# Optimization experiments

Hardware: AMD Instinct MI355X
Metric: run time of the kernel (lower is better)

Reference implementation:

```python
import jax, jax.numpy as jnp
import numpy as np

K, P, Q, D = 16, 1024, 1024, 64  # heads, value-in dim, out dim, head dim; P'=P, Q'=Q, D'=D
B, N = 2, 2048                   # batch, seq (self-attention: M=N)
TEMPERATURE = jnp.sqrt(jnp.float32(D))

def _xavier(key, shape):
    fan_in, fan_out = shape[-2], shape[-1]
    lim = jnp.sqrt(6.0 / (fan_in + fan_out))
    return jax.random.uniform(key, shape, jnp.float32, -lim, lim)

def setup_inputs() -> dict:
    key = jax.random.key(0)
    k0, k1, k2, k3, k4 = jax.random.split(key, 5)
    return {
        'y_prime': jax.random.normal(k0, (B, N, Q), jnp.float32),
        'mask': jnp.zeros((N, N), jnp.float32),  # log-domain additive mask [M,N]
        'Lam_x': _xavier(k1, (K, P, D)),  # Lambda^(x): [K,P',D']
        'Lam_y': _xavier(k2, (K, Q, D)),  # Lambda^(y): [K,Q',D']
        'Th_x': _xavier(k3, (K, P, D)),   # Theta^(x):  [K,P,D]
        'Th_y': _xavier(k4, (K, Q, D)),   # Theta^(y):  [K,Q,D]
    }

def reference(y_prime, mask, Lam_x, Lam_y, Th_x, Th_y):
    # self-attention: x' = x = y'
    x_p = y_prime
    x = x_p
    # key projection: [B,M,K,D']
    r = jnp.einsum('bmp,kpd->bmkd', x_p, Lam_x)
    # bilinear scores: [K,B,M,N]
    r = jnp.einsum('bmkd,kqd,bnq->kbmn', r, Lam_y, y_prime)
    r = r + mask[None, None, :, :]
    # softmax over M (axis=-2), scaled by sqrt(D')
    A = jax.nn.softmax(r / TEMPERATURE, axis=-2)
    # value aggregation: [B,N,K,D]
    r = jnp.einsum('kbmn,bmp,kpd->bnkd', A, x, Th_x)
    # output projection: [B,N,Q]
    return jnp.einsum('bnkd,kqd->bnq', r, Th_y)
```

## Files before the change

### kernel.cpp

```cpp
#include <hip/hip_runtime.h>
#include <hip/hip_bf16.h>

#define KH 16
#define PD 1024
#define QD 1024
#define DD 64
#define BB 2
#define NN 2048
#define BN 4096
#define ST 72
#define SOFT_C 12.0f

typedef unsigned short u16;
typedef __attribute__((ext_vector_type(8))) short bf16x8;
typedef __attribute__((ext_vector_type(4))) short bf16x4;
typedef __attribute__((ext_vector_type(4))) float f32x4;

__device__ __forceinline__ float bf2f(u16 u) {
    return __uint_as_float(((unsigned)u) << 16);
}
__device__ __forceinline__ u16 f2bf(float f) {
    unsigned x = __float_as_uint(f);
    x += 0x7FFFu + ((x >> 16) & 1u);
    return (u16)(x >> 16);
}
__device__ __forceinline__ f32x4 mfma_k32(bf16x8 a, bf16x8 b, f32x4 c) {
    return __builtin_amdgcn_mfma_f32_16x16x32_bf16(a, b, c, 0, 0, 0);
}
__device__ __forceinline__ f32x4 mfma_k16(bf16x4 a, bf16x4 b, f32x4 c) {
#if __has_builtin(__builtin_amdgcn_mfma_f32_16x16x16bf16_1k)
    return __builtin_amdgcn_mfma_f32_16x16x16bf16_1k(a, b, c, 0, 0, 0);
#else
    asm("v_mfma_f32_16x16x16_bf16 %0, %1, %2, %0" : "+v"(c) : "v"(a), "v"(b));
    return c;
#endif
}
__device__ __forceinline__ bf16x8 ldfrag(const u16* base, int r0, int kc, int lane) {
    return *reinterpret_cast<const bf16x8*>(base + (r0 + (lane & 15)) * ST + kc +
                                            ((lane >> 4) << 3));
}
__device__ __forceinline__ bf16x4 ldfrag4(const u16* base, int r0, int kc, int lane) {
    return *reinterpret_cast<const bf16x4*>(base + (r0 + (lane & 15)) * ST + kc +
                                            ((lane >> 4) << 2));
}
__device__ __forceinline__ bf16x8 ldfragL(const u16* base, int r0, int kc, int lane) {
    return *reinterpret_cast<const bf16x8*>(base + ((r0 + (lane & 15)) << 6) + kc +
                                            ((lane >> 4) << 3));
}
__device__ __forceinline__ bf16x4 pack4(float a, float b, float c, float d) {
    union { bf16x4 v; __hip_bfloat162 h[2]; } u;
    u.h[0] = __float22bfloat162_rn(make_float2(a, b));
    u.h[1] = __float22bfloat162_rn(make_float2(c, d));
    return u.v;
}
__device__ __forceinline__ void gl_lds16(const u16* g, u16* l) {
    __builtin_amdgcn_global_load_lds(
        (const __attribute__((address_space(1))) void*)g,
        (__attribute__((address_space(3))) void*)l, 16, 0, 0);
}
template <int ROWS>
__device__ __forceinline__ void stage_dma(const u16* __restrict__ src, int ld,
                                          u16* dst, int lane, int w) {
#pragma unroll
    for (int c = 0; c < ROWS / 32; ++c) {
        int rbase = (w * (ROWS / 32) + c) * 8;
        const u16* g = src + (size_t)(rbase + (lane >> 3)) * ld + ((lane & 7) << 3);
        gl_lds16(g, dst + (rbase << 6));
    }
}
template <int ROWS, int NT>
__device__ __forceinline__ void stage_rows(const u16* __restrict__ src, int ld,
                                           u16* dst, int tid) {
#pragma unroll
    for (int it = 0; it < ROWS * 8 / NT; ++it) {
        int chunk = it * NT + tid;
        int row = chunk >> 3, col = (chunk & 7) << 3;
        *reinterpret_cast<uint4*>(dst + row * ST + col) =
            *reinterpret_cast<const uint4*>(src + row * ld + col);
    }
}

__global__ void detect_kernel(const u16* __restrict__ y, int* flag, int* mnz) {
    __shared__ int cnt;
    if (threadIdx.x == 0) cnt = 0;
    __syncthreads();
    int local = 0;
    for (int i = threadIdx.x; i < 8192; i += 256) {
        u16 u = y[i];
        int e = (u >> 7) & 0xFF;
        if (u == 0 || (e >= 96 && e < 160)) local++;
    }
    atomicAdd(&cnt, local);
    __syncthreads();
    if (threadIdx.x == 0) {
        *flag = (cnt > 7372) ? 1 : 0;
        *mnz = 0;
    }
}

__global__ __launch_bounds__(256) void prep_kernel(
    const void* __restrict__ ysrc, const void* __restrict__ msrc,
    const void* __restrict__ s0, const void* __restrict__ s1,
    const void* __restrict__ s2, const void* __restrict__ s3,
    u16* __restrict__ ycan, u16* __restrict__ LamXt, u16* __restrict__ LamYt,
    u16* __restrict__ ThXt, u16* __restrict__ ThYr, u16* __restrict__ maskc,
    const int* __restrict__ flag, int* __restrict__ mnz) {
    int z = blockIdx.z, bx = blockIdx.x, tid = threadIdx.x;
    int isbf = *flag;
    if (z == 0) {
        size_t n4 = (size_t)NN * NN / 8;
        if (!isbf) n4 *= 2;
        const uint4* p = (const uint4*)msrc;
        unsigned acc = 0;
        for (size_t i = (size_t)bx * 256 + tid; i < n4; i += 256 * 256) {
            uint4 v = p[i];
            acc |= v.x | v.y | v.z | v.w;
        }
        if (acc) atomicOr(mnz, 1);
    } else if (z == 1) {
        int n = BN * PD;
        for (int i = (bx * 256 + tid) * 4; i < n; i += 256 * 256 * 4) {
            if (isbf) {
                *reinterpret_cast<uint2*>(ycan + i) =
                    *reinterpret_cast<const uint2*>((const u16*)ysrc + i);
            } else {
                float4 f = *reinterpret_cast<const float4*>((const float*)ysrc + i);
                u16 t[4] = {f2bf(f.x), f2bf(f.y), f2bf(f.z), f2bf(f.w)};
                *reinterpret_cast<uint2*>(ycan + i) = *reinterpret_cast<uint2*>(t);
            }
        }
    } else if (z <= 4) {
        const void* src = (z == 2) ? s0 : (z == 3) ? s1 : s2;
        u16* dst = (z == 2) ? LamXt : (z == 3) ? LamYt : ThXt;
        float scale = (z == 3) ? 0.125f : 1.0f;
        int k = bx >> 4, p0 = (bx & 15) * 64;
        __shared__ float T[64][65];
        const u16* s16 = (const u16*)src + ((size_t)k * PD + p0) * DD;
        const float* s32 = (const float*)src + ((size_t)k * PD + p0) * DD;
#pragma unroll
        for (int it = 0; it < 2; ++it) {
            int chunk = it * 256 + tid;
            int row = chunk >> 3, c8 = (chunk & 7) << 3;
            float f[8];
            if (isbf) {
                uint4 v = *reinterpret_cast<const uint4*>(s16 + row * DD + c8);
                u16 t[8];
                *reinterpret_cast<uint4*>(t) = v;
#pragma unroll
                for (int e = 0; e < 8; ++e) f[e] = bf2f(t[e]);
            } else {
                float4 a = *reinterpret_cast<const float4*>(s32 + row * DD + c8);
                float4 b = *reinterpret_cast<const float4*>(s32 + row * DD + c8 + 4);
                f[0] = a.x; f[1] = a.y; f[2] = a.z; f[3] = a.w;
                f[4] = b.x; f[5] = b.y; f[6] = b.z; f[7] = b.w;
            }
#pragma unroll
            for (int e = 0; e < 8; ++e) T[row][c8 + e] = f[e] * scale;
        }
        __syncthreads();
        u16* drow = dst + (size_t)k * DD * PD + p0;
#pragma unroll
        for (int it = 0; it < 2; ++it) {
            int chunk = it * 256 + tid;
            int d = chunk >> 3, c8 = (chunk & 7) << 3;
            u16 t[8];
#pragma unroll
            for (int e = 0; e < 8; ++e) t[e] = f2bf(T[c8 + e][d]);
            *reinterpret_cast<uint4*>(drow + (size_t)d * PD + c8) =
                *reinterpret_cast<uint4*>(t);
        }
    } else if (z == 5) {
        int k = bx >> 4, q0 = (bx & 15) * 64;
#pragma unroll
        for (int it = 0; it < 2; ++it) {
            int chunk = it * 256 + tid;
            int row = chunk >> 3, c8 = (chunk & 7) << 3;
            size_t si = ((size_t)k * QD + q0 + row) * DD + c8;
            u16 t[8];
            if (isbf) {
                *reinterpret_cast<uint4*>(t) =
                    *reinterpret_cast<const uint4*>((const u16*)s3 + si);
            } else {
                float4 a = *reinterpret_cast<const float4*>((const float*)s3 + si);
                float4 b = *reinterpret_cast<const float4*>((const float*)s3 + si + 4);
                t[0] = f2bf(a.x); t[1] = f2bf(a.y); t[2] = f2bf(a.z); t[3] = f2bf(a.w);
                t[4] = f2bf(b.x); t[5] = f2bf(b.y); t[6] = f2bf(b.z); t[7] = f2bf(b.w);
            }
            *reinterpret_cast<uint4*>(ThYr + (size_t)(q0 + row) * (KH * DD) +
                                      k * DD + c8) = *reinterpret_cast<uint4*>(t);
        }
    } else {
        size_t n8 = (size_t)NN * NN / 8;
        for (size_t c = (size_t)bx * 256 + tid; c < n8; c += 256 * 256) {
            size_t i = c * 8;
            float f[8];
            if (isbf) {
                uint4 v = *reinterpret_cast<const uint4*>((const u16*)msrc + i);
                u16 t[8];
                *reinterpret_cast<uint4*>(t) = v;
#pragma unroll
                for (int e = 0; e < 8; ++e) f[e] = bf2f(t[e]);
            } else {
                float4 a = *reinterpret_cast<const float4*>((const float*)msrc + i);
                float4 b = *reinterpret_cast<const float4*>((const float*)msrc + i + 4);
                f[0] = a.x; f[1] = a.y; f[2] = a.z; f[3] = a.w;
                f[4] = b.x; f[5] = b.y; f[6] = b.z; f[7] = b.w;
            }
            u16 t[8];
#pragma unroll
            for (int e = 0; e < 8; ++e) t[e] = f2bf(f[e] * 0.125f);
            *reinterpret_cast<uint4*>(maskc + i) = *reinterpret_cast<uint4*>(t);
        }
    }
}

__global__ __launch_bounds__(256, 3) void proj_gemm(
    const u16* __restrict__ A,
    const u16* __restrict__ Bm,
    u16* __restrict__ Xk, u16* __restrict__ Yk, u16* __restrict__ Vtg) {
    int tid = threadIdx.x, lane = tid & 63, w = tid >> 6;
    int mhalf = w & 1, nhalf = w >> 1;
    int m0 = blockIdx.x * 128, n0 = blockIdx.y * 128;
    __shared__ u16 As[128 * 64];
    __shared__ u16 Bs[128 * 64];
    f32x4 acc[4][4] = {};

    for (int kk = 0; kk < PD; kk += 64) {
        __syncthreads();
        stage_dma<128>(A + (size_t)m0 * PD + kk, PD, As, lane, w);
        stage_dma<128>(Bm + (size_t)n0 * PD + kk, PD, Bs, lane, w);
        __syncthreads();
#pragma unroll
        for (int kc = 0; kc < 64; kc += 32) {
            bf16x8 af[4], bf[4];
#pragma unroll
            for (int i = 0; i < 4; ++i) af[i] = ldfragL(As, mhalf * 64 + i * 16, kc, lane);
#pragma unroll
            for (int j = 0; j < 4; ++j) bf[j] = ldfragL(Bs, nhalf * 64 + j * 16, kc, lane);
#pragma unroll
            for (int i = 0; i < 4; ++i)
#pragma unroll
                for (int j = 0; j < 4; ++j) acc[i][j] = mfma_k32(af[i], bf[j], acc[i][j]);
        }
    }
    int s = n0 >> 10;
    int quad = lane >> 4, col = lane & 15;
    u16* stg = nhalf ? Bs : As;
    __syncthreads();
    if (s == 2) {
#pragma unroll
        for (int i = 0; i < 4; ++i)
#pragma unroll
            for (int j = 0; j < 4; ++j)
                *reinterpret_cast<bf16x4*>(stg + (j * 16 + col) * 128 + mhalf * 64 +
                                           i * 16 + quad * 4) =
                    pack4(acc[i][j][0], acc[i][j][1], acc[i][j][2], acc[i][j][3]);
    } else {
#pragma unroll
        for (int i = 0; i < 4; ++i)
#pragma unroll
            for (int j = 0; j < 4; ++j)
#pragma unroll
                for (int reg = 0; reg < 4; ++reg)
                    stg[(mhalf * 64 + i * 16 + quad * 4 + reg) * 64 + j * 16 + col] =
                        f2bf(acc[i][j][reg]);
    }
    __syncthreads();
#pragma unroll
    for (int h = 0; h < 2; ++h) {
        int kh = ((n0 + h * 64) >> 6) & 15;
        const u16* src = h ? Bs : As;
        if (s == 2) {
            u16* vb = Vtg + (size_t)kh * DD * BN + m0;
#pragma unroll
            for (int it = 0; it < 4; ++it) {
                int chunk = it * 256 + tid;
                int d = chunk >> 4, off = (chunk & 15) * 8;
                *reinterpret_cast<uint4*>(vb + (size_t)d * BN + off) =
                    *reinterpret_cast<const uint4*>(src + d * 128 + off);
            }
        } else {
            u16* ob = (s == 0 ? Xk : Yk) + (size_t)kh * BN * DD + (size_t)m0 * DD;
#pragma unroll
            for (int it = 0; it < 4; ++it) {
                int chunk = it * 256 + tid;
                *reinterpret_cast<uint4*>(ob + chunk * 8) =
                    *reinterpret_cast<const uint4*>(src + chunk * 8);
            }
        }
    }
}

__global__ __launch_bounds__(256, 4) void attn_kernel(
    const u16* __restrict__ Xk,
    const u16* __restrict__ Yk,
    const u16* __restrict__ Vtg,
    const u16* __restrict__ maskc,
    const int* __restrict__ mnz,
    u16* __restrict__ O) {
    int tid = threadIdx.x, lane = tid & 63, w = tid >> 6;
    int quad = lane >> 4, col = lane & 15;
    int q0 = blockIdx.x * 128, k = blockIdx.y, b = blockIdx.z;
    const u16* Qp = Yk + ((size_t)k * BN + b * NN + q0) * DD;
    const u16* Kp = Xk + ((size_t)k * BN + b * NN) * DD;
    const u16* Vp = Vtg + (size_t)k * DD * BN + b * NN;
    __shared__ u16 Qs[128 * ST];
    __shared__ u16 Ks[64 * ST];
    __shared__ u16 Vt[64 * ST];
    int mz = *mnz;

    stage_rows<128, 256>(Qp, DD, Qs, tid);
    __syncthreads();
    bf16x8 qf[2][2];
#pragma unroll
    for (int g = 0; g < 2; ++g)
#pragma unroll
        for (int kc = 0; kc < 2; ++kc)
            qf[g][kc] = ldfrag(Qs, w * 32 + g * 16, kc * 32, lane);

    float lp[2] = {0.0f, 0.0f};
    f32x4 oacc[2][4] = {};

    for (int m0 = 0; m0 < NN; m0 += 64) {
        __syncthreads();
        stage_rows<64, 256>(Kp + (size_t)m0 * DD, DD, Ks, tid);
        stage_rows<64, 256>(Vp + m0, BN, Vt, tid);
        __syncthreads();

        f32x4 sacc[2][4] = {};
#pragma unroll
        for (int kg = 0; kg < 4; ++kg) {
            bf16x8 a0 = ldfrag(Ks, kg * 16, 0, lane);
            bf16x8 a1 = ldfrag(Ks, kg * 16, 32, lane);
#pragma unroll
            for (int g = 0; g < 2; ++g) {
                sacc[g][kg] = mfma_k32(a0, qf[g][0], sacc[g][kg]);
                sacc[g][kg] = mfma_k32(a1, qf[g][1], sacc[g][kg]);
            }
        }
        if (mz) {
#pragma unroll
            for (int g = 0; g < 2; ++g)
#pragma unroll
                for (int kg = 0; kg < 4; ++kg)
#pragma unroll
                    for (int reg = 0; reg < 4; ++reg)
                        sacc[g][kg][reg] += bf2f(
                            maskc[(size_t)(m0 + kg * 16 + quad * 4 + reg) * NN +
                                  q0 + w * 32 + g * 16 + col]);
        }
        bf16x4 pb[2][4];
#pragma unroll
        for (int g = 0; g < 2; ++g)
#pragma unroll
            for (int kg = 0; kg < 4; ++kg) {
                float p0 = __expf(sacc[g][kg][0] - SOFT_C);
                float p1 = __expf(sacc[g][kg][1] - SOFT_C);
                float p2 = __expf(sacc[g][kg][2] - SOFT_C);
                float p3 = __expf(sacc[g][kg][3] - SOFT_C);
                lp[g] += (p0 + p1) + (p2 + p3);
                pb[g][kg] = pack4(p0, p1, p2, p3);
            }
#pragma unroll
        for (int kg = 0; kg < 4; ++kg)
#pragma unroll
            for (int dg = 0; dg < 4; ++dg) {
                bf16x4 av = ldfrag4(Vt, dg * 16, kg * 16, lane);
#pragma unroll
                for (int g = 0; g < 2; ++g)
                    oacc[g][dg] = mfma_k16(av, pb[g][kg], oacc[g][dg]);
            }
    }

    float inv[2];
#pragma unroll
    for (int g = 0; g < 2; ++g) {
        float l = lp[g];
        l += __shfl_xor(l, 16);
        l += __shfl_xor(l, 32);
        inv[g] = 1.0f / l;
    }
#pragma unroll
    for (int g = 0; g < 2; ++g)
#pragma unroll
        for (int dg = 0; dg < 4; ++dg)
            *reinterpret_cast<bf16x4*>(Qs + (w * 32 + g * 16 + col) * ST + dg * 16 +
                                       quad * 4) =
                pack4(oacc[g][dg][0] * inv[g], oacc[g][dg][1] * inv[g],
                      oacc[g][dg][2] * inv[g], oacc[g][dg][3] * inv[g]);
    __syncthreads();
    int r = tid >> 1, h = tid & 1;
    const u16* srow = Qs + r * ST + h * 32;
    u16* drow = O + (size_t)(b * NN + q0 + r) * (KH * DD) + k * DD + h * 32;
#pragma unroll
    for (int u = 0; u < 4; ++u)
        *reinterpret_cast<uint4*>(drow + u * 8) =
            *reinterpret_cast<const uint4*>(srow + u * 8);
}

__global__ __launch_bounds__(256, 3) void out_gemm(
    const u16* __restrict__ A,
    const u16* __restrict__ Bm,
    const int* __restrict__ flag,
    void* __restrict__ outv) {
    int tid = threadIdx.x, lane = tid & 63, w = tid >> 6;
    int mhalf = w & 1, nhalf = w >> 1;
    int m0 = blockIdx.x * 128, n0 = blockIdx.y * 128;
    __shared__ u16 As[128 * 64];
    __shared__ u16 Bs[128 * 64];
    f32x4 acc[4][4] = {};

    for (int kk = 0; kk < KH * DD; kk += 64) {
        __syncthreads();
        stage_dma<128>(A + (size_t)m0 * (KH * DD) + kk, KH * DD, As, lane, w);
        stage_dma<128>(Bm + (size_t)n0 * (KH * DD) + kk, KH * DD, Bs, lane, w);
        __syncthreads();
#pragma unroll
        for (int kc = 0; kc < 64; kc += 32) {
            bf16x8 af[4], bf[4];
#pragma unroll
            for (int i = 0; i < 4; ++i) af[i] = ldfragL(As, mhalf * 64 + i * 16, kc, lane);
#pragma unroll
            for (int j = 0; j < 4; ++j) bf[j] = ldfragL(Bs, nhalf * 64 + j * 16, kc, lane);
#pragma unroll
            for (int i = 0; i < 4; ++i)
#pragma unroll
                for (int j = 0; j < 4; ++j) acc[i][j] = mfma_k32(af[i], bf[j], acc[i][j]);
        }
    }
    int isbf = *flag;
    int quad = lane >> 4, col = lane & 15;
#pragma unroll
    for (int i = 0; i < 4; ++i)
#pragma unroll
        for (int j = 0; j < 4; ++j)
#pragma unroll
            for (int reg = 0; reg < 4; ++reg) {
                size_t row = m0 + mhalf * 64 + i * 16 + quad * 4 + reg;
                int c = n0 + nhalf * 64 + j * 16 + col;
                if (isbf)
                    ((u16*)outv)[row * QD + c] = f2bf(acc[i][j][reg]);
                else
                    ((float*)outv)[row * QD + c] = acc[i][j][reg];
            }
}

extern "C" void kernel_launch(void* const* d_in, const int* in_sizes, int n_in,
                              void* d_out, int out_size, void* d_ws, size_t ws_size,
                              hipStream_t stream) {
    char* wsb = (char*)d_ws;
    int* flag = (int*)wsb;
    int* mnz = (int*)(wsb + 16);
    u16* ycan = (u16*)(wsb + 64);
    const size_t NYP = (size_t)BN * PD;
    const size_t NW = (size_t)KH * PD * DD;
    const size_t OSZ = (size_t)BN * KH * DD;
    u16* Wcat = ycan + NYP;
    u16* ThYr = Wcat + 3 * NW;
    u16* Xk = ThYr + NW;
    u16* Yk = Xk + OSZ;
    u16* Vtg = Yk + OSZ;
    u16* maskc = Vtg + OSZ;
    u16* Ob = ycan;

    detect_kernel<<<1, 256, 0, stream>>>((const u16*)d_in[0], flag, mnz);
    prep_kernel<<<dim3(256, 1, 7), 256, 0, stream>>>(
        d_in[0], d_in[1], d_in[2], d_in[3], d_in[4], d_in[5], ycan, Wcat,
        Wcat + NW, Wcat + 2 * NW, ThYr, maskc, flag, mnz);
    proj_gemm<<<dim3(BN / 128, 3072 / 128), 256, 0, stream>>>(ycan, Wcat, Xk, Yk, Vtg);
    attn_kernel<<<dim3(NN / 128, KH, BB), 256, 0, stream>>>(Xk, Yk, Vtg, maskc,
                                                            mnz, Ob);
    out_gemm<<<dim3(BN / 128, QD / 128), 256, 0, stream>>>(Ob, ThYr, flag, d_out);
}
```

Measured before the change: 242.0 us.

## Triple-buffer attention K/V tiles with 512 threads; stage fp32 output through LDS

The attention kernel moves from 256 to 512 threads per block. Each wave now owns 16 query rows instead of 32, and K/V tiles go through a triple-buffered LDS ring fed by register prefetch two tiles ahead, so there is one barrier per tile instead of two. The output GEMM's fp32 path now stages accumulators through shared memory so it can write coalesced float4 rows instead of scattered scalar stores. In exchange, launch bounds of (512,1) may limit occupancy, each wave reuses K fragments less, and the epilogue adds extra barriers.

```diff
diff --git a/kernel.cpp b/kernel.cpp
--- a/kernel.cpp
+++ b/kernel.cpp
@@ -291,7 +291,7 @@
     }
 }
 
-__global__ __launch_bounds__(256, 4) void attn_kernel(
+__global__ __launch_bounds__(512, 1) void attn_kernel(
     const u16* __restrict__ Xk,
     const u16* __restrict__ Yk,
     const u16* __restrict__ Vtg,
@@ -305,97 +305,102 @@
     const u16* Kp = Xk + ((size_t)k * BN + b * NN) * DD;
     const u16* Vp = Vtg + (size_t)k * DD * BN + b * NN;
     __shared__ u16 Qs[128 * ST];
-    __shared__ u16 Ks[64 * ST];
-    __shared__ u16 Vt[64 * ST];
+    __shared__ u16 Kb[3][64 * ST];
+    __shared__ u16 Vb[3][64 * ST];
     int mz = *mnz;
 
-    stage_rows<128, 256>(Qp, DD, Qs, tid);
+    stage_rows<128, 512>(Qp, DD, Qs, tid);
+
+    int srow = tid >> 3, scol = (tid & 7) << 3;
+    const u16* kgp = Kp + (size_t)srow * DD + scol;
+    const u16* vgp = Vp + (size_t)srow * BN + scol;
+    int soff = srow * ST + scol;
+
+    uint4 kr = *reinterpret_cast<const uint4*>(kgp);
+    uint4 vr = *reinterpret_cast<const uint4*>(vgp);
+    *reinterpret_cast<uint4*>(Kb[0] + soff) = kr;
+    *reinterpret_cast<uint4*>(Vb[0] + soff) = vr;
+    kr = *reinterpret_cast<const uint4*>(kgp + (size_t)64 * DD);
+    vr = *reinterpret_cast<const uint4*>(vgp + 64);
     __syncthreads();
-    bf16x8 qf[2][2];
-#pragma unroll
-    for (int g = 0; g < 2; ++g)
-#pragma unroll
-        for (int kc = 0; kc < 2; ++kc)
-            qf[g][kc] = ldfrag(Qs, w * 32 + g * 16, kc * 32, lane);
-
-    float lp[2] = {0.0f, 0.0f};
-    f32x4 oacc[2][4] = {};
-
-    for (int m0 = 0; m0 < NN; m0 += 64) {
-        __syncthreads();
-        stage_rows<64, 256>(Kp + (size_t)m0 * DD, DD, Ks, tid);
-        stage_rows<64, 256>(Vp + m0, BN, Vt, tid);
-        __syncthreads();
-
-        f32x4 sacc[2][4] = {};
+
+    bf16x8 qf0 = ldfrag(Qs, w * 16, 0, lane);
+    bf16x8 qf1 = ldfrag(Qs, w * 16, 32, lane);
+
+    float lp = 0.0f;
+    f32x4 oacc[4] = {};
+
+    for (int t = 0; t < 32; ++t) {
+        int cur = t % 3;
+        if (t < 31) {
+            int nxt = (t + 1) % 3;
+            *reinterpret_cast<uint4*>(Kb[nxt] + soff) = kr;
+            *reinterpret_cast<uint4*>(Vb[nxt] + soff) = vr;
+            if (t < 30) {
+                kr = *reinterpret_cast<const uint4*>(kgp + (size_t)(t + 2) * 64 * DD);
+                vr = *reinterpret_cast<const uint4*>(vgp + (t + 2) * 64);
+            }
+            __syncthreads();
+        }
+        const u16* Ks = Kb[cur];
+        const u16* Vt = Vb[cur];
+        int m0 = t * 64;
+
+        f32x4 sacc[4] = {};
 #pragma unroll
         for (int kg = 0; kg < 4; ++kg) {
             bf16x8 a0 = ldfrag(Ks, kg * 16, 0, lane);
             bf16x8 a1 = ldfrag(Ks, kg * 16, 32, lane);
-#pragma unroll
-            for (int g = 0; g < 2; ++g) {
-                sacc[g][kg] = mfma_k32(a0, qf[g][0], sacc[g][kg]);
-                sacc[g][kg] = mfma_k32(a1, qf[g][1], sacc[g][kg]);
-            }
+            sacc[kg] = mfma_k32(a0, qf0, sacc[kg]);
+            sacc[kg] = mfma_k32(a1, qf1, sacc[kg]);
         }
         if (mz) {
 #pragma unroll
-            for (int g = 0; g < 2; ++g)
-#pragma unroll
-                for (int kg = 0; kg < 4; ++kg)
-#pragma unroll
-                    for (int reg = 0; reg < 4; ++reg)
-                        sacc[g][kg][reg] += bf2f(
-                            maskc[(size_t)(m0 + kg * 16 + quad * 4 + reg) * NN +
-                                  q0 + w * 32 + g * 16 + col]);
-        }
-        bf16x4 pb[2][4];
-#pragma unroll
-        for (int g = 0; g < 2; ++g)
-#pragma unroll
-            for (int kg = 0; kg < 4; ++kg) {
-                float p0 = __expf(sacc[g][kg][0] - SOFT_C);
-                float p1 = __expf(sacc[g][kg][1] - SOFT_C);
-                float p2 = __expf(sacc[g][kg][2] - SOFT_C);
-                float p3 = __expf(sacc[g][kg][3] - SOFT_C);
-                lp[g] += (p0 + p1) + (p2 + p3);
-                pb[g][kg] = pack4(p0, p1, p2, p3);
-            }
+            for (int kg = 0; kg < 4; ++kg)
+#pragma unroll
+                for (int reg = 0; reg < 4; ++reg)
+                    sacc[kg][reg] += bf2f(
+                        maskc[(size_t)(m0 + kg * 16 + quad * 4 + reg) * NN + q0 +
+                              w * 16 + col]);
+        }
+        bf16x4 pb[4];
+#pragma unroll
+        for (int kg = 0; kg < 4; ++kg) {
+            float p0 = __expf(sacc[kg][0] - SOFT_C);
+            float p1 = __expf(sacc[kg][1] - SOFT_C);
+            float p2 = __expf(sacc[kg][2] - SOFT_C);
+            float p3 = __expf(sacc[kg][3] - SOFT_C);
+            lp += (p0 + p1) + (p2 + p3);
+            pb[kg] = pack4(p0, p1, p2, p3);
+        }
 #pragma unroll
         for (int kg = 0; kg < 4; ++kg)
 #pragma unroll
             for (int dg = 0; dg < 4; ++dg) {
                 bf16x4 av = ldfrag4(Vt, dg * 16, kg * 16, lane);
-#pragma unroll
-                for (int g = 0; g < 2; ++g)
-                    oacc[g][dg] = mfma_k16(av, pb[g][kg], oacc[g][dg]);
-            }
-    }
-
-    float inv[2];
-#pragma unroll
-    for (int g = 0; g < 2; ++g) {
-        float l = lp[g];
-        l += __shfl_xor(l, 16);
-        l += __shfl_xor(l, 32);
-        inv[g] = 1.0f / l;
-    }
-#pragma unroll
-    for (int g = 0; g < 2; ++g)
-#pragma unroll
-        for (int dg = 0; dg < 4; ++dg)
-            *reinterpret_cast<bf16x4*>(Qs + (w * 32 + g * 16 + col) * ST + dg * 16 +
-                                       quad * 4) =
-                pack4(oacc[g][dg][0] * inv[g], oacc[g][dg][1] * inv[g],
-                      oacc[g][dg][2] * inv[g], oacc[g][dg][3] * inv[g]);
+                oacc[dg] = mfma_k16(av, pb[kg], oacc[dg]);
+            }
+    }
+
+    float l = lp;
+    l += __shfl_xor(l, 16);
+    l += __shfl_xor(l, 32);
+    float inv = 1.0f / l;
+
+#pragma unroll
+    for (int dg = 0; dg < 4; ++dg)
+        *reinterpret_cast<bf16x4*>(Qs + (w * 16 + col) * ST + dg * 16 + quad * 4) =
+            pack4(oacc[dg][0] * inv, oacc[dg][1] * inv, oacc[dg][2] * inv,
+                  oacc[dg][3] * inv);
     __syncthreads();
-    int r = tid >> 1, h = tid & 1;
-    const u16* srow = Qs + r * ST + h * 32;
-    u16* drow = O + (size_t)(b * NN + q0 + r) * (KH * DD) + k * DD + h * 32;
-#pragma unroll
-    for (int u = 0; u < 4; ++u)
-        *reinterpret_cast<uint4*>(drow + u * 8) =
-            *reinterpret_cast<const uint4*>(srow + u * 8);
+#pragma unroll
+    for (int it = 0; it < 2; ++it) {
+        int chunk = it * 512 + tid;
+        int row = chunk >> 3, c8 = (chunk & 7) << 3;
+        *reinterpret_cast<uint4*>(O + (size_t)(b * NN + q0 + row) * (KH * DD) +
+                                  k * DD + c8) =
+            *reinterpret_cast<const uint4*>(Qs + row * ST + c8);
+    }
 }
 
 __global__ __launch_bounds__(256, 3) void out_gemm(
@@ -406,8 +411,9 @@
     int tid = threadIdx.x, lane = tid & 63, w = tid >> 6;
     int mhalf = w & 1, nhalf = w >> 1;
     int m0 = blockIdx.x * 128, n0 = blockIdx.y * 128;
-    __shared__ u16 As[128 * 64];
-    __shared__ u16 Bs[128 * 64];
+    __shared__ u16 S[2][128 * 64];
+    u16* As = S[0];
+    u16* Bs = S[1];
     f32x4 acc[4][4] = {};
 
     for (int kk = 0; kk < KH * DD; kk += 64) {
@@ -430,19 +436,43 @@
     }
     int isbf = *flag;
     int quad = lane >> 4, col = lane & 15;
-#pragma unroll
-    for (int i = 0; i < 4; ++i)
-#pragma unroll
-        for (int j = 0; j < 4; ++j)
-#pragma unroll
-            for (int reg = 0; reg < 4; ++reg) {
-                size_t row = m0 + mhalf * 64 + i * 16 + quad * 4 + reg;
-                int c = n0 + nhalf * 64 + j * 16 + col;
-                if (isbf)
+    if (isbf) {
+#pragma unroll
+        for (int i = 0; i < 4; ++i)
+#pragma unroll
+            for (int j = 0; j < 4; ++j)
+#pragma unroll
+                for (int reg = 0; reg < 4; ++reg) {
+                    size_t row = m0 + mhalf * 64 + i * 16 + quad * 4 + reg;
+                    int c = n0 + nhalf * 64 + j * 16 + col;
                     ((u16*)outv)[row * QD + c] = f2bf(acc[i][j][reg]);
-                else
-                    ((float*)outv)[row * QD + c] = acc[i][j][reg];
-            }
+                }
+    } else {
+        float* Sf = (float*)&S[0][0];
+#pragma unroll
+        for (int h = 0; h < 2; ++h) {
+            __syncthreads();
+            if (mhalf == h) {
+#pragma unroll
+                for (int i = 0; i < 4; ++i)
+#pragma unroll
+                    for (int j = 0; j < 4; ++j)
+#pragma unroll
+                        for (int reg = 0; reg < 4; ++reg)
+                            Sf[(i * 16 + quad * 4 + reg) * 128 + nhalf * 64 +
+                               j * 16 + col] = acc[i][j][reg];
+            }
+            __syncthreads();
+            float* orow = (float*)outv + (size_t)(m0 + h * 64) * QD + n0;
+#pragma unroll
+            for (int it = 0; it < 8; ++it) {
+                int chunk = it * 256 + tid;
+                int row = chunk >> 5, c4 = (chunk & 31) * 4;
+                *reinterpret_cast<float4*>(orow + (size_t)row * QD + c4) =
+                    *reinterpret_cast<const float4*>(Sf + row * 128 + c4);
+            }
+        }
+    }
 }
 
 extern "C" void kernel_launch(void* const* d_in, const int* in_sizes, int n_in,
@@ -468,7 +498,7 @@
         d_in[0], d_in[1], d_in[2], d_in[3], d_in[4], d_in[5], ycan, Wcat,
         Wcat + NW, Wcat + 2 * NW, ThYr, maskc, flag, mnz);
     proj_gemm<<<dim3(BN / 128, 3072 / 128), 256, 0, stream>>>(ycan, Wcat, Xk, Yk, Vtg);
-    attn_kernel<<<dim3(NN / 128, KH, BB), 256, 0, stream>>>(Xk, Yk, Vtg, maskc,
+    attn_kernel<<<dim3(NN / 128, KH, BB), 512, 0, stream>>>(Xk, Yk, Vtg, maskc,
                                                             mnz, Ob);
     out_gemm<<<dim3(BN / 128, QD / 128), 256, 0, stream>>>(Ob, ThYr, flag, d_out);
 }
```

Result: faster. 235.3 us (-2.8%).
